# Performance work log

Measured on AMD Instinct MI355X. Metric: run time of the kernel, lower is better.

Reference implementation:

```python
import jax, jax.numpy as jnp
import numpy as np

# NF4 codebook (bitsandbytes nf4 data type, 16 levels)
NF4_TABLE = np.array([
    -1.0, -0.6961928009986877, -0.5250730514526367, -0.39491748809814453,
    -0.28444138169288635, -0.18477343022823334, -0.09105003625154495, 0.0,
    0.07958029955625534, 0.16093020141124725, 0.24611230194568634,
    0.33791524171829224, 0.44070982933044434, 0.5626170039176941,
    0.7229568362236023, 1.0], dtype=np.float32)

BLOCKSIZE = 64
SCALING = 32.0 / 16.0  # lora_alpha / r


def setup_inputs() -> dict:
    key = jax.random.key(0)
    k1, k2, k3, k4, k5 = jax.random.split(key, 5)
    tokens, in_f, out_f, r = 256, 4096, 11008, 16
    x = jax.random.normal(k1, (tokens, in_f), dtype=jnp.float32)
    q_codes = jax.random.randint(k2, (out_f, in_f), 0, 16, dtype=jnp.int32)
    absmax = jax.random.uniform(k3, (out_f, in_f // BLOCKSIZE), dtype=jnp.float32)
    lora_A = jax.random.normal(k4, (r, in_f), dtype=jnp.float32) * (1.0 / np.sqrt(in_f))
    lora_B = jax.random.normal(k5, (out_f, r), dtype=jnp.float32) * 0.02
    return {"x": x, "q_codes": q_codes, "absmax": absmax,
            "lora_A": lora_A, "lora_B": lora_B}


def reference(x, q_codes, absmax, lora_A, lora_B):
    out_f, in_f = q_codes.shape
    nf4 = jnp.asarray(NF4_TABLE, dtype=x.dtype)
    # Dequantize: codebook lookup, then per-block absmax scale.
    W = nf4[q_codes].reshape(out_f, in_f // BLOCKSIZE, BLOCKSIZE)
    W = (W * absmax[:, :, None]).reshape(out_f, in_f)  # [out_f, in_f]
    # Base 4-bit linear (no bias in bnb Linear4bit default here).
    base = x @ W.T  # [tokens, out_f]
    # LoRA path: dropout p=0 is identity in eval; scaling = alpha/r.
    lora = (x @ lora_A.T) @ lora_B.T  # [tokens, r] -> [tokens, out_f]
    return base + lora * jnp.asarray(SCALING, dtype=x.dtype)
```

## Files before the change

### kernel.cpp

```cpp
#include <hip/hip_runtime.h>
#include <hip/hip_fp16.h>

typedef unsigned int uint;
typedef unsigned short ushort;

typedef __attribute__((ext_vector_type(8))) _Float16 f16x8;
typedef __attribute__((ext_vector_type(4))) float f32x4;

#define TOK 256
#define OUTF 11008
#define INF 4096
#define BM 256
#define BN 64
#define NT2 172

__device__ __constant__ float NF4_TBL[16] = {
    -1.0f, -0.6961928009986877f, -0.5250730514526367f, -0.39491748809814453f,
    -0.28444138169288635f, -0.18477343022823334f, -0.09105003625154495f, 0.0f,
    0.07958029955625534f, 0.16093020141124725f, 0.24611230194568634f,
    0.33791524171829224f, 0.44070982933044434f, 0.5626170039176941f,
    0.7229568362236023f, 1.0f};

__device__ __forceinline__ ushort f2h(float f) {
  return __half_as_ushort(__float2half(f));
}

__device__ __forceinline__ void async_cp16(const void* g, void* l) {
  __builtin_amdgcn_global_load_lds(
      (const __attribute__((address_space(1))) uint*)g,
      (__attribute__((address_space(3))) uint*)l, 16, 0, 0);
}

__device__ __forceinline__ float nf4v(int c, int tbits) {
  return __int_as_float(__builtin_amdgcn_ds_bpermute(c << 2, tbits));
}

__device__ __forceinline__ void step_barrier() {
  asm volatile("s_waitcnt lgkmcnt(0)" ::: "memory");
  __builtin_amdgcn_s_barrier();
}

__global__ void prep_kernel(const float* __restrict__ x, uint4* __restrict__ xf4,
                            const float4* __restrict__ lB4, ushort4* __restrict__ lBh4,
                            const int4* __restrict__ qc4, uint* __restrict__ q4) {
  const int stride = gridDim.x * blockDim.x;
  const int t0 = blockIdx.x * blockDim.x + threadIdx.x;
  for (int i = t0; i < OUTF * (INF / 8); i += stride) {
    int4 a = qc4[(size_t)i * 2];
    int4 b = qc4[(size_t)i * 2 + 1];
    uint p = (uint)(a.x & 15) | ((uint)(a.y & 15) << 4) | ((uint)(a.z & 15) << 8) |
             ((uint)(a.w & 15) << 12) | ((uint)(b.x & 15) << 16) |
             ((uint)(b.y & 15) << 20) | ((uint)(b.z & 15) << 24) |
             ((uint)(b.w & 15) << 28);
    q4[i] = p;
  }
  for (int f = t0; f < TOK * INF / 8; f += stride) {
    int l = f & 63;
    int rlo = l & 15, chunk = l >> 4;
    int ms = (f >> 6) & 7;
    int mt = ms >> 1, ks2 = ms & 1;
    int w = (f >> 9) & 3;
    int kb = f >> 11;
    int m = w * 64 + mt * 16 + rlo;
    int k0 = kb * 64 + (ks2 * 4 + chunk) * 8;
    const float4* src = (const float4*)(x + (size_t)m * INF + k0);
    float4 v0 = src[0], v1 = src[1];
    union { ushort4 h[2]; uint4 u; } pk;
    pk.h[0].x = f2h(v0.x); pk.h[0].y = f2h(v0.y); pk.h[0].z = f2h(v0.z); pk.h[0].w = f2h(v0.w);
    pk.h[1].x = f2h(v1.x); pk.h[1].y = f2h(v1.y); pk.h[1].z = f2h(v1.z); pk.h[1].w = f2h(v1.w);
    xf4[f] = pk.u;
  }
  for (int i = t0; i < OUTF * 16; i += stride) {
    int n = i >> 4, jq = i & 15;
    ushort4 o = {0, 0, 0, 0};
    if (jq < 4) {
      float4 v = lB4[n * 4 + jq];
      o.x = f2h(v.x); o.y = f2h(v.y); o.z = f2h(v.z); o.w = f2h(v.w);
    }
    lBh4[i] = o;
  }
}

__global__ __launch_bounds__(1024)
void xa_kernel(const float* __restrict__ x, const float* __restrict__ lA,
               ushort* __restrict__ xa2) {
  const int m = blockIdx.x;
  const int t = threadIdx.x;
  const float4* x4 = (const float4*)(x + (size_t)m * INF);
  const float4* lA4 = (const float4*)lA;
  float4 xv = x4[t];
  float acc[16];
#pragma unroll
  for (int j = 0; j < 16; ++j) {
    float4 a = lA4[j * (INF / 4) + t];
    acc[j] = xv.x * a.x + xv.y * a.y + xv.z * a.z + xv.w * a.w;
  }
#pragma unroll
  for (int j = 0; j < 16; ++j)
#pragma unroll
    for (int s = 32; s > 0; s >>= 1) acc[j] += __shfl_xor(acc[j], s, 64);
  __shared__ float red[16][16];
  const int w = t >> 6, l = t & 63;
  if (l == 0) {
#pragma unroll
    for (int j = 0; j < 16; ++j) red[w][j] = acc[j];
  }
  __syncthreads();
  if (t < 64) {
    ushort v = 0;
    if (t < 16) {
      float s = 0.f;
#pragma unroll
      for (int w2 = 0; w2 < 16; ++w2) s += red[w2][t];
      v = f2h(2.0f * s);
    }
    xa2[m * 64 + t] = v;
  }
}

__global__ __launch_bounds__(256, 2)
void gemm_kernel(const uint* __restrict__ q4, const float* __restrict__ am,
                 const ushort* __restrict__ xf, const ushort* __restrict__ lBh,
                 const ushort* __restrict__ xa2, float* __restrict__ dest, int nst) {
  __shared__ ushort Bbuf[2][64 * 64];
  __shared__ float Qax[4096];

  const int tid = threadIdx.x;
  const int w = tid >> 6;
  const int l = tid & 63;
  const int chunk = l >> 4;
  const int rlo = l & 15;
  const int split = blockIdx.x / NT2;
  const int ntile = blockIdx.x - split * NT2;
  const int n0 = ntile * BN;
  const int kb0 = split * nst;

  const int tbits = __float_as_int(NF4_TBL[l & 15]);

  const int qr = tid >> 2;
  const int oc2 = (tid & 3) << 1;
  const uint* qb = q4 + (size_t)(n0 + qr) * (INF / 8) + (size_t)kb0 * 8 + oc2;
  const int bd0 = qr * 64 + ((oc2 ^ (qr & 7)) << 3);
  const int bd1 = qr * 64 + (((oc2 + 1) ^ (qr & 7)) << 3);

  int boff[2][4];
#pragma unroll
  for (int ks2 = 0; ks2 < 2; ++ks2)
#pragma unroll
    for (int nt = 0; nt < 4; ++nt)
      boff[ks2][nt] = (nt * 16 + rlo) * 64 + (((ks2 * 4 + chunk) ^ (rlo & 7)) << 3);

  f32x4 acc[4][4];
#pragma unroll
  for (int mt = 0; mt < 4; ++mt)
#pragma unroll
    for (int nt = 0; nt < 4; ++nt) acc[mt][nt] = (f32x4){0.f, 0.f, 0.f, 0.f};

  auto loadA = [&](f16x8 ar[2][4], int kb) {
    const ushort* base = xf + ((size_t)kb * 4 + w) * 4096 + (size_t)l * 8;
#pragma unroll
    for (int mt = 0; mt < 4; ++mt)
#pragma unroll
      for (int ks2 = 0; ks2 < 2; ++ks2)
        ar[ks2][mt] = *(const f16x8*)(base + (mt * 2 + ks2) * 512);
  };

  auto dequantF = [&](uint2 q, int kbt, ushort* bb) {
    const __half2 ax2 = __float2half2_rn(Qax[(kbt >> 2) * 256 + qr * 4 + (kbt & 3)]);
    const uint q0 = q.x, q1 = q.y;
    union { __half2 h[4]; uint4 u; } r0, r1;
    r0.h[0] = __hmul2(__floats2half2_rn(nf4v(q0 & 15, tbits), nf4v((q0 >> 4) & 15, tbits)), ax2);
    r0.h[1] = __hmul2(__floats2half2_rn(nf4v((q0 >> 8) & 15, tbits), nf4v((q0 >> 12) & 15, tbits)), ax2);
    r0.h[2] = __hmul2(__floats2half2_rn(nf4v((q0 >> 16) & 15, tbits), nf4v((q0 >> 20) & 15, tbits)), ax2);
    r0.h[3] = __hmul2(__floats2half2_rn(nf4v((q0 >> 24) & 15, tbits), nf4v(q0 >> 28, tbits)), ax2);
    r1.h[0] = __hmul2(__floats2half2_rn(nf4v(q1 & 15, tbits), nf4v((q1 >> 4) & 15, tbits)), ax2);
    r1.h[1] = __hmul2(__floats2half2_rn(nf4v((q1 >> 8) & 15, tbits), nf4v((q1 >> 12) & 15, tbits)), ax2);
    r1.h[2] = __hmul2(__floats2half2_rn(nf4v((q1 >> 16) & 15, tbits), nf4v((q1 >> 20) & 15, tbits)), ax2);
    r1.h[3] = __hmul2(__floats2half2_rn(nf4v((q1 >> 24) & 15, tbits), nf4v(q1 >> 28, tbits)), ax2);
    *(uint4*)&bb[bd0] = r0.u;
    *(uint4*)&bb[bd1] = r1.u;
  };

  auto compute = [&](f16x8 ar[2][4], const ushort* bb) {
    __builtin_amdgcn_s_setprio(1);
#pragma unroll
    for (int ks2 = 0; ks2 < 2; ++ks2) {
      f16x8 b[4];
#pragma unroll
      for (int nt = 0; nt < 4; ++nt) b[nt] = *(const f16x8*)&bb[boff[ks2][nt]];
#pragma unroll
      for (int mt = 0; mt < 4; ++mt)
#pragma unroll
        for (int nt = 0; nt < 4; ++nt)
          acc[mt][nt] = __builtin_amdgcn_mfma_f32_16x16x32_f16(ar[ks2][mt], b[nt], acc[mt][nt], 0, 0, 0);
    }
    __builtin_amdgcn_s_setprio(0);
  };

  if (w == 0) {
#pragma unroll
    for (int j = 0; j < 16; ++j)
      async_cp16(am + (size_t)(n0 + l) * 64 + j * 4, (char*)Qax + j * 1024);
  }
  f16x8 arA[2][4], arB[2][4];
  loadA(arA, kb0);
  loadA(arB, kb0 + 1);
  uint2 qA = *(const uint2*)qb;
  uint2 qB = *(const uint2*)(qb + 8);
  __syncthreads();
  dequantF(qA, kb0, Bbuf[0]);
  step_barrier();

  for (int s = 0; s < nst; s += 2) {
    compute(arA, Bbuf[0]);
    if (s + 1 < nst) dequantF(qB, kb0 + s + 1, Bbuf[1]);
    if (s + 2 < nst) {
      loadA(arA, kb0 + s + 2);
      qA = *(const uint2*)(qb + (size_t)(s + 2) * 8);
    }
    step_barrier();
    compute(arB, Bbuf[1]);
    if (s + 2 < nst) dequantF(qA, kb0 + s + 2, Bbuf[0]);
    if (s + 3 < nst) {
      loadA(arB, kb0 + s + 3);
      qB = *(const uint2*)(qb + (size_t)(s + 3) * 8);
    }
    step_barrier();
  }

  if (split == 0) {
    f16x8 a_l[4], b_l[4];
#pragma unroll
    for (int mt = 0; mt < 4; ++mt)
      a_l[mt] = *(const f16x8*)(xa2 + (size_t)(w * 64 + mt * 16 + rlo) * 64 + chunk * 8);
#pragma unroll
    for (int nt = 0; nt < 4; ++nt)
      b_l[nt] = *(const f16x8*)(lBh + (size_t)(n0 + nt * 16 + rlo) * 64 + chunk * 8);
#pragma unroll
    for (int mt = 0; mt < 4; ++mt)
#pragma unroll
      for (int nt = 0; nt < 4; ++nt)
        acc[mt][nt] = __builtin_amdgcn_mfma_f32_16x16x32_f16(a_l[mt], b_l[nt], acc[mt][nt], 0, 0, 0);
  }

  float* dst = dest + (size_t)split * TOK * OUTF;
#pragma unroll
  for (int mt = 0; mt < 4; ++mt) {
#pragma unroll
    for (int nt = 0; nt < 4; ++nt) {
      int c = n0 + nt * 16 + rlo;
#pragma unroll
      for (int r = 0; r < 4; ++r) {
        int row = w * 64 + mt * 16 + chunk * 4 + r;
        dst[(size_t)row * OUTF + c] = acc[mt][nt][r];
      }
    }
  }
}

__global__ void reduce_kernel(const float4* __restrict__ part, float4* __restrict__ out,
                              int ks) {
  const int QN = TOK * OUTF / 4;
  int i = blockIdx.x * blockDim.x + threadIdx.x;
  if (i < QN) {
    float4 s = part[i];
    for (int s2 = 1; s2 < ks; ++s2) {
      float4 p = part[(size_t)s2 * QN + i];
      s.x += p.x; s.y += p.y; s.z += p.z; s.w += p.w;
    }
    out[i] = s;
  }
}

extern "C" void kernel_launch(void* const* d_in, const int* in_sizes, int n_in,
                              void* d_out, int out_size, void* d_ws, size_t ws_size,
                              hipStream_t stream) {
  const float* x = (const float*)d_in[0];
  const int* qc = (const int*)d_in[1];
  const float* am = (const float*)d_in[2];
  const float* lA = (const float*)d_in[3];
  const float* lB = (const float*)d_in[4];
  float* out = (float*)d_out;

  const size_t off_lB = (size_t)TOK * INF * 2;
  const size_t off_xa2 = off_lB + (size_t)OUTF * 64 * 2;
  const size_t off_q4 = off_xa2 + (size_t)TOK * 64 * 2;
  const size_t off_part = off_q4 + (size_t)OUTF * (INF / 8) * 4;
  const size_t part_bytes = (size_t)TOK * OUTF * 4;

  ushort* xf = (ushort*)d_ws;
  ushort* lBh = (ushort*)((char*)d_ws + off_lB);
  ushort* xa2 = (ushort*)((char*)d_ws + off_xa2);
  uint* q4 = (uint*)((char*)d_ws + off_q4);
  float* part = (float*)((char*)d_ws + off_part);

  int ks = 1;
  if (ws_size >= off_part + 4 * part_bytes) ks = 4;
  else if (ws_size >= off_part + 2 * part_bytes) ks = 2;
  float* dest = (ks == 1) ? out : part;

  prep_kernel<<<2048, 256, 0, stream>>>(x, (uint4*)xf, (const float4*)lB,
                                        (ushort4*)lBh, (const int4*)qc, q4);
  xa_kernel<<<TOK, 1024, 0, stream>>>(x, lA, xa2);
  gemm_kernel<<<NT2 * ks, 256, 0, stream>>>(q4, am, xf, lBh, xa2, dest, 64 / ks);
  if (ks > 1)
    reduce_kernel<<<(TOK * OUTF / 4 + 255) / 256, 256, 0, stream>>>((const float4*)part,
                                                                    (float4*)out, ks);
}
```

Before: 327.4 us.

## Read int32 NF4 codes directly in GEMM instead of prepacking to nibbles

Drops the prep pass that packed the int32 codes into 4-bit nibbles. The GEMM kernel now loads the raw int32 codes (four int4 loads per thread per k-step) and dequantizes them straight into the LDS tile. This saves one full read of the 180MB code array plus the packed write and re-read. In exchange each GEMM block reads 8x more code bytes, and with a k-split every code is still read once in total. The code mask `& 15` is also dropped, which relies on inputs staying within 0..15.

```diff
diff --git a/kernel.cpp b/kernel.cpp
--- a/kernel.cpp
+++ b/kernel.cpp
@@ -35,25 +35,25 @@
   return __int_as_float(__builtin_amdgcn_ds_bpermute(c << 2, tbits));
 }
 
+__device__ __forceinline__ uint2 dq4(int4 c, __half2 ax2, int tbits) {
+  __half2 h0 = __floats2half2_rn(nf4v(c.x, tbits), nf4v(c.y, tbits));
+  __half2 h1 = __floats2half2_rn(nf4v(c.z, tbits), nf4v(c.w, tbits));
+  h0 = __hmul2(h0, ax2);
+  h1 = __hmul2(h1, ax2);
+  union { __half2 h[2]; uint2 u; } r;
+  r.h[0] = h0; r.h[1] = h1;
+  return r.u;
+}
+
 __device__ __forceinline__ void step_barrier() {
   asm volatile("s_waitcnt lgkmcnt(0)" ::: "memory");
   __builtin_amdgcn_s_barrier();
 }
 
 __global__ void prep_kernel(const float* __restrict__ x, uint4* __restrict__ xf4,
-                            const float4* __restrict__ lB4, ushort4* __restrict__ lBh4,
-                            const int4* __restrict__ qc4, uint* __restrict__ q4) {
+                            const float4* __restrict__ lB4, ushort4* __restrict__ lBh4) {
   const int stride = gridDim.x * blockDim.x;
   const int t0 = blockIdx.x * blockDim.x + threadIdx.x;
-  for (int i = t0; i < OUTF * (INF / 8); i += stride) {
-    int4 a = qc4[(size_t)i * 2];
-    int4 b = qc4[(size_t)i * 2 + 1];
-    uint p = (uint)(a.x & 15) | ((uint)(a.y & 15) << 4) | ((uint)(a.z & 15) << 8) |
-             ((uint)(a.w & 15) << 12) | ((uint)(b.x & 15) << 16) |
-             ((uint)(b.y & 15) << 20) | ((uint)(b.z & 15) << 24) |
-             ((uint)(b.w & 15) << 28);
-    q4[i] = p;
-  }
   for (int f = t0; f < TOK * INF / 8; f += stride) {
     int l = f & 63;
     int rlo = l & 15, chunk = l >> 4;
@@ -119,7 +119,7 @@
 }
 
 __global__ __launch_bounds__(256, 2)
-void gemm_kernel(const uint* __restrict__ q4, const float* __restrict__ am,
+void gemm_kernel(const int* __restrict__ qc, const float* __restrict__ am,
                  const ushort* __restrict__ xf, const ushort* __restrict__ lBh,
                  const ushort* __restrict__ xa2, float* __restrict__ dest, int nst) {
   __shared__ ushort Bbuf[2][64 * 64];
@@ -137,11 +137,16 @@
 
   const int tbits = __float_as_int(NF4_TBL[l & 15]);
 
-  const int qr = tid >> 2;
-  const int oc2 = (tid & 3) << 1;
-  const uint* qb = q4 + (size_t)(n0 + qr) * (INF / 8) + (size_t)kb0 * 8 + oc2;
-  const int bd0 = qr * 64 + ((oc2 ^ (qr & 7)) << 3);
-  const int bd1 = qr * 64 + (((oc2 + 1) ^ (qr & 7)) << 3);
+  const int qrg = tid >> 4;
+  const int qch = tid & 15;
+  const int* qbase[4];
+  int bdst[4];
+#pragma unroll
+  for (int p = 0; p < 4; ++p) {
+    int r = p * 16 + qrg;
+    qbase[p] = qc + (size_t)(n0 + r) * INF + kb0 * 64 + qch * 4;
+    bdst[p] = r * 64 + (((qch >> 1) ^ (r & 7)) << 3) + (qch & 1) * 4;
+  }
 
   int boff[2][4];
 #pragma unroll
@@ -165,20 +170,18 @@
         ar[ks2][mt] = *(const f16x8*)(base + (mt * 2 + ks2) * 512);
   };
 
-  auto dequantF = [&](uint2 q, int kbt, ushort* bb) {
-    const __half2 ax2 = __float2half2_rn(Qax[(kbt >> 2) * 256 + qr * 4 + (kbt & 3)]);
-    const uint q0 = q.x, q1 = q.y;
-    union { __half2 h[4]; uint4 u; } r0, r1;
-    r0.h[0] = __hmul2(__floats2half2_rn(nf4v(q0 & 15, tbits), nf4v((q0 >> 4) & 15, tbits)), ax2);
-    r0.h[1] = __hmul2(__floats2half2_rn(nf4v((q0 >> 8) & 15, tbits), nf4v((q0 >> 12) & 15, tbits)), ax2);
-    r0.h[2] = __hmul2(__floats2half2_rn(nf4v((q0 >> 16) & 15, tbits), nf4v((q0 >> 20) & 15, tbits)), ax2);
-    r0.h[3] = __hmul2(__floats2half2_rn(nf4v((q0 >> 24) & 15, tbits), nf4v(q0 >> 28, tbits)), ax2);
-    r1.h[0] = __hmul2(__floats2half2_rn(nf4v(q1 & 15, tbits), nf4v((q1 >> 4) & 15, tbits)), ax2);
-    r1.h[1] = __hmul2(__floats2half2_rn(nf4v((q1 >> 8) & 15, tbits), nf4v((q1 >> 12) & 15, tbits)), ax2);
-    r1.h[2] = __hmul2(__floats2half2_rn(nf4v((q1 >> 16) & 15, tbits), nf4v((q1 >> 20) & 15, tbits)), ax2);
-    r1.h[3] = __hmul2(__floats2half2_rn(nf4v((q1 >> 24) & 15, tbits), nf4v(q1 >> 28, tbits)), ax2);
-    *(uint4*)&bb[bd0] = r0.u;
-    *(uint4*)&bb[bd1] = r1.u;
+  auto loadQ = [&](int4 q[4], int s) {
+#pragma unroll
+    for (int p = 0; p < 4; ++p) q[p] = *(const int4*)(qbase[p] + (size_t)s * 64);
+  };
+
+  auto dequantF = [&](int4 q[4], int kbt, ushort* bb) {
+#pragma unroll
+    for (int p = 0; p < 4; ++p) {
+      int r = p * 16 + qrg;
+      __half2 ax2 = __float2half2_rn(Qax[(kbt >> 2) * 256 + r * 4 + (kbt & 3)]);
+      *(uint2*)&bb[bdst[p]] = dq4(q[p], ax2, tbits);
+    }
   };
 
   auto compute = [&](f16x8 ar[2][4], const ushort* bb) {
@@ -203,10 +206,11 @@
       async_cp16(am + (size_t)(n0 + l) * 64 + j * 4, (char*)Qax + j * 1024);
   }
   f16x8 arA[2][4], arB[2][4];
+  int4 qA[4], qB[4];
   loadA(arA, kb0);
   loadA(arB, kb0 + 1);
-  uint2 qA = *(const uint2*)qb;
-  uint2 qB = *(const uint2*)(qb + 8);
+  loadQ(qA, 0);
+  loadQ(qB, 1);
   __syncthreads();
   dequantF(qA, kb0, Bbuf[0]);
   step_barrier();
@@ -216,14 +220,14 @@
     if (s + 1 < nst) dequantF(qB, kb0 + s + 1, Bbuf[1]);
     if (s + 2 < nst) {
       loadA(arA, kb0 + s + 2);
-      qA = *(const uint2*)(qb + (size_t)(s + 2) * 8);
+      loadQ(qA, s + 2);
     }
     step_barrier();
     compute(arB, Bbuf[1]);
     if (s + 2 < nst) dequantF(qA, kb0 + s + 2, Bbuf[0]);
     if (s + 3 < nst) {
       loadA(arB, kb0 + s + 3);
-      qB = *(const uint2*)(qb + (size_t)(s + 3) * 8);
+      loadQ(qB, s + 3);
     }
     step_barrier();
   }
@@ -284,14 +288,12 @@
 
   const size_t off_lB = (size_t)TOK * INF * 2;
   const size_t off_xa2 = off_lB + (size_t)OUTF * 64 * 2;
-  const size_t off_q4 = off_xa2 + (size_t)TOK * 64 * 2;
-  const size_t off_part = off_q4 + (size_t)OUTF * (INF / 8) * 4;
+  const size_t off_part = off_xa2 + (size_t)TOK * 64 * 2;
   const size_t part_bytes = (size_t)TOK * OUTF * 4;
 
   ushort* xf = (ushort*)d_ws;
   ushort* lBh = (ushort*)((char*)d_ws + off_lB);
   ushort* xa2 = (ushort*)((char*)d_ws + off_xa2);
-  uint* q4 = (uint*)((char*)d_ws + off_q4);
   float* part = (float*)((char*)d_ws + off_part);
 
   int ks = 1;
@@ -300,9 +302,9 @@
   float* dest = (ks == 1) ? out : part;
 
   prep_kernel<<<2048, 256, 0, stream>>>(x, (uint4*)xf, (const float4*)lB,
-                                        (ushort4*)lBh, (const int4*)qc, q4);
+                                        (ushort4*)lBh);
   xa_kernel<<<TOK, 1024, 0, stream>>>(x, lA, xa2);
-  gemm_kernel<<<NT2 * ks, 256, 0, stream>>>(q4, am, xf, lBh, xa2, dest, 64 / ks);
+  gemm_kernel<<<NT2 * ks, 256, 0, stream>>>(qc, am, xf, lBh, xa2, dest, 64 / ks);
   if (ks > 1)
     reduce_kernel<<<(TOK * OUTF / 4 + 255) / 256, 256, 0, stream>>>((const float4*)part,
                                                                     (float4*)out, ks);
```

After: 318.2 us. 2.8% less time.
